# Kernel tuning notes

Measured on AMD Instinct MI355X. Metric: run time of the kernel, lower is better.

The kernel has to match this reference:

```python
import jax, jax.numpy as jnp
import numpy as np

R = 32
EPS = 0.0
BN_EPS = 1e-5


def _voxelize(features, idx):
    # features: [C, N], idx: [N] int32 flat voxel index in [0, R^3)
    V = R * R * R
    pts = features.T  # [N, C]
    sums = jax.ops.segment_sum(pts, idx, num_segments=V)          # [V, C]
    cnts = jax.ops.segment_sum(jnp.ones_like(idx, jnp.float32), idx, num_segments=V)  # [V]
    avg = sums / jnp.maximum(cnts, 1.0)[:, None]
    mx = jax.ops.segment_max(pts, idx, num_segments=V)            # [V, C], -inf for empty
    mx = jnp.where(cnts[:, None] > 0, mx, 0.0)
    return avg, mx, cnts


def reference(features, coords, conv_w, conv_b, bn_gamma, bn_beta, bn_mean, bn_var):
    B, C, N = features.shape
    # --- coordinate normalization (coords detached in original) ---
    nc = coords - jnp.mean(coords, axis=2, keepdims=True)          # [B,3,N]
    norms = jnp.linalg.norm(nc, axis=1, keepdims=True)             # [B,1,N]
    denom = jnp.max(norms, axis=2, keepdims=True) * 2.0 + EPS      # [B,1,1]
    nc = nc / denom + 0.5
    nc = jnp.clip(nc * R, 0.0, R - 1)                              # [B,3,N]
    vox = jnp.round(nc).astype(jnp.int32)                          # [B,3,N]
    idx = vox[:, 0] * (R * R) + vox[:, 1] * R + vox[:, 2]          # [B,N]
    # --- dual scatter reduction (avg + max) per batch ---
    avg, mx, _ = jax.vmap(_voxelize)(features, idx)                # [B, V, C] each
    fea = jnp.concatenate([mx, avg], axis=-1)                      # [B, V, 2C]
    # --- 1x1 Conv3d == channel matmul ---
    y = jnp.einsum('bvc,oc->bvo', fea, conv_w) + conv_b            # [B, V, C]
    # --- BatchNorm3d (eval mode) ---
    y = (y - bn_mean) * (bn_gamma / jnp.sqrt(bn_var + BN_EPS)) + bn_beta
    # --- Swish ---
    y = y * jax.nn.sigmoid(y)
    out = jnp.transpose(y, (0, 2, 1)).reshape(B, C, R, R, R)
    return out, nc


def setup_inputs() -> dict:
    key = jax.random.key(0)
    ks = jax.random.split(key, 8)
    B, C, N = 8, 240, 16384
    return {
        'features': jax.random.normal(ks[0], (B, C, N), jnp.float32),
        'coords': jax.random.normal(ks[1], (B, 3, N), jnp.float32),
        'conv_w': jax.random.normal(ks[2], (C, 2 * C), jnp.float32) * 0.05,
        'conv_b': jax.random.normal(ks[3], (C,), jnp.float32) * 0.05,
        'bn_gamma': jnp.ones((C,), jnp.float32),
        'bn_beta': jnp.zeros((C,), jnp.float32),
        'bn_mean': jnp.zeros((C,), jnp.float32),
        'bn_var': jax.random.uniform(ks[4], (C,), jnp.float32, 0.5, 1.5),
    }
```

## Files before the change

### kernel.cpp

```cpp
#include <hip/hip_runtime.h>
#include <math.h>

#define RR 32
#define V 32768
#define C 240
#define N 16384
#define B 8
#define K2C 480
#define NCOL 1024
#define FPAD 488
#define EBUF 512

typedef __attribute__((ext_vector_type(8))) short bf16x8;
typedef __attribute__((ext_vector_type(4))) float f32x4;

__device__ __forceinline__ unsigned short f2bf(float x) {
    unsigned u = __float_as_uint(x);
    u += 0x7fffu + ((u >> 16) & 1u);
    return (unsigned short)(u >> 16);
}

__global__ __launch_bounds__(1024) void stats_kernel(const float* __restrict__ coords,
                                                     float* __restrict__ stats,
                                                     int* __restrict__ hist,
                                                     const float* __restrict__ w,
                                                     unsigned short* __restrict__ w_bf) {
    int b = blockIdx.x, tid = threadIdx.x;
    int4 z4 = {0, 0, 0, 0};
    int4* hz = (int4*)(hist + b * V);
    for (int i = tid; i < V / 4; i += 1024) hz[i] = z4;
    for (int i = tid; i < 14400; i += 1024) {
        int g = b * 14400 + i;
        w_bf[g] = f2bf(w[g]);
    }
    const float* cb = coords + (size_t)b * 3 * N;
    __shared__ float red[1024];
    float m[3];
    for (int d = 0; d < 3; ++d) {
        float s = 0.f;
        for (int n = tid; n < N; n += 1024) s += cb[d * N + n];
        red[tid] = s; __syncthreads();
        for (int w2 = 512; w2 > 0; w2 >>= 1) { if (tid < w2) red[tid] += red[tid + w2]; __syncthreads(); }
        m[d] = red[0] / (float)N;
        __syncthreads();
    }
    float mx = 0.f;
    for (int n = tid; n < N; n += 1024) {
        float dx = cb[0 * N + n] - m[0];
        float dy = cb[1 * N + n] - m[1];
        float dz = cb[2 * N + n] - m[2];
        mx = fmaxf(mx, dx * dx + dy * dy + dz * dz);
    }
    red[tid] = mx; __syncthreads();
    for (int w2 = 512; w2 > 0; w2 >>= 1) { if (tid < w2) red[tid] = fmaxf(red[tid], red[tid + w2]); __syncthreads(); }
    if (tid == 0) {
        stats[b * 4 + 0] = m[0];
        stats[b * 4 + 1] = m[1];
        stats[b * 4 + 2] = m[2];
        stats[b * 4 + 3] = 2.f * sqrtf(red[0]);
    }
}

__global__ __launch_bounds__(256) void nc_idx_kernel(const float* __restrict__ coords,
                                                     const float* __restrict__ stats,
                                                     float* __restrict__ nc_out,
                                                     int* __restrict__ idxbuf,
                                                     int* __restrict__ hist) {
    int t = blockIdx.x * 256 + threadIdx.x;
    int b = t >> 14;
    int n = t & (N - 1);
    float denom = stats[b * 4 + 3];
    int v[3];
#pragma unroll
    for (int d = 0; d < 3; ++d) {
        float x = coords[((size_t)b * 3 + d) * N + n];
        float t0 = (x - stats[b * 4 + d]) / denom + 0.5f;
        t0 = t0 * (float)RR;
        t0 = fminf(fmaxf(t0, 0.f), (float)(RR - 1));
        nc_out[((size_t)b * 3 + d) * N + n] = t0;
        v[d] = (int)rintf(t0);
    }
    int iv = v[0] * (RR * RR) + v[1] * RR + v[2];
    idxbuf[t] = iv;
    atomicAdd(hist + b * V + iv, 1);
}

__global__ __launch_bounds__(1024) void prefix_kernel(const int* __restrict__ hist,
                                                      int* __restrict__ starts,
                                                      int* __restrict__ cursor) {
    __shared__ int part[1024];
    int b = blockIdx.x, t = threadIdx.x;
    int base = b * V + t * 32;
    const int4* hp = (const int4*)(hist + base);
    int4 h[8];
    int s = 0;
#pragma unroll
    for (int j = 0; j < 8; ++j) { h[j] = hp[j]; s += h[j].x + h[j].y + h[j].z + h[j].w; }
    part[t] = s; __syncthreads();
    for (int off = 1; off < 1024; off <<= 1) {
        int x = (t >= off) ? part[t - off] : 0;
        __syncthreads();
        part[t] += x;
        __syncthreads();
    }
    int run = part[t] - s;
    int4* sp = (int4*)(starts + base);
    int4* cp = (int4*)(cursor + base);
#pragma unroll
    for (int j = 0; j < 8; ++j) {
        int4 o;
        o.x = run; run += h[j].x;
        o.y = run; run += h[j].y;
        o.z = run; run += h[j].z;
        o.w = run; run += h[j].w;
        sp[j] = o; cp[j] = o;
    }
}

__global__ __launch_bounds__(256) void plist_kernel(const int* __restrict__ idxbuf,
                                                    int* __restrict__ cursor,
                                                    int* __restrict__ ptlist) {
    int t = blockIdx.x * 256 + threadIdx.x;
    int b = t >> 14;
    int n = t & (N - 1);
    int iv = idxbuf[t];
    int pos = atomicAdd(cursor + b * V + iv, 1);
    ptlist[(b << 14) + pos] = (n << 5) | (iv & 31);
}

__global__ __launch_bounds__(256) void transpose_kernel(const float* __restrict__ feat,
                                                        unsigned short* __restrict__ featT) {
    __shared__ float t[C][33];
    int b = blockIdx.y;
    int n0 = blockIdx.x * 32;
    int l = threadIdx.x;
    const float* fb = feat + (size_t)b * C * N;
    unsigned short* fTb = featT + (size_t)b * N * C;
    int nl = l & 31, cs = l >> 5;
#pragma unroll
    for (int p = 0; p < 30; ++p) {
        int c = p * 8 + cs;
        t[c][nl] = fb[(size_t)c * N + n0 + nl];
    }
    __syncthreads();
    int ci = l & 127;
    int nh = l >> 7;
#pragma unroll
    for (int p = 0; p < 16; ++p) {
        int n = 2 * p + nh;
        if (ci < 120) {
            unsigned lo = f2bf(t[2 * ci][n]);
            unsigned hi = f2bf(t[2 * ci + 1][n]);
            *(unsigned*)&fTb[(size_t)(n0 + n) * C + 2 * ci] = lo | (hi << 16);
        }
    }
}

__global__ __launch_bounds__(256) void column_kernel(
    const unsigned short* __restrict__ featT,
    const int* __restrict__ ptlist,
    const int* __restrict__ starts,
    const int* __restrict__ hist,
    const unsigned short* __restrict__ w_bf,
    const float* __restrict__ cbias, const float* __restrict__ gamma,
    const float* __restrict__ beta, const float* __restrict__ mean,
    const float* __restrict__ var,
    float* __restrict__ out) {
    const int col = blockIdx.x, b = blockIdx.y;
    const int tid = threadIdx.x;
    const int v0 = col * 32;
    float* outb = out + (size_t)b * C * V;

    __shared__ float A_s[C], B_s[C];
    __shared__ unsigned short fea_s[32][FPAD];
    __shared__ int cnt_s[32];
    __shared__ int ebuf[EBUF];

    if (tid < C) {
        float sc = gamma[tid] * rsqrtf(var[tid] + 1e-5f);
        A_s[tid] = sc;
        B_s[tid] = (cbias[tid] - mean[tid]) * sc + beta[tid];
    }
    if (tid < 32) cnt_s[tid] = hist[b * V + v0 + tid];
    __syncthreads();

    int pc = 0;
#pragma unroll
    for (int z = 0; z < 32; ++z) pc += cnt_s[z];

    if (pc == 0) {
        for (int i = tid; i < C * 32; i += 256) {
            int o = i >> 5, vv = i & 31;
            float y = B_s[o];
            y = y / (1.f + __expf(-y));
            outb[(size_t)o * V + v0 + vv] = y;
        }
        return;
    }

    for (int i = tid; i < 32 * FPAD / 2; i += 256) ((unsigned*)fea_s)[i] = 0u;

    const int cu = tid;
    const bool act = tid < 120;
    const int pos = starts[b * V + v0];
    const int* pl = ptlist + (b << 14) + pos;
    const unsigned short* fT = featT + (size_t)b * N * C;

    float s0 = 0.f, s1 = 0.f, mx0 = -INFINITY, mx1 = -INFINITY;
    int curz = -1;
    for (int base = 0; base < pc; base += EBUF) {
        int mm = min(EBUF, pc - base);
        __syncthreads();
        for (int i = tid; i < mm; i += 256) ebuf[i] = pl[base + i];
        __syncthreads();
        if (act) {
            for (int i0 = 0; i0 < mm; i0 += 16) {
                int m = min(16, mm - i0);
                int e_[16];
#pragma unroll
                for (int j = 0; j < 16; ++j) e_[j] = ebuf[i0 + ((j < m) ? j : m - 1)];
                unsigned u_[16];
#pragma unroll
                for (int j = 0; j < 16; ++j)
                    u_[j] = *(const unsigned*)&fT[(size_t)(e_[j] >> 5) * C + 2 * cu];
#pragma unroll
                for (int j = 0; j < 16; ++j) {
                    if (j < m) {
                        int zj = e_[j] & 31;
                        if (zj != curz) {
                            if (curz >= 0) {
                                float k = (float)cnt_s[curz];
                                unsigned pm = (unsigned)f2bf(mx0) | ((unsigned)f2bf(mx1) << 16);
                                unsigned pa = (unsigned)f2bf(s0 / k) | ((unsigned)f2bf(s1 / k) << 16);
                                *(unsigned*)&fea_s[curz][2 * cu] = pm;
                                *(unsigned*)&fea_s[curz][C + 2 * cu] = pa;
                            }
                            curz = zj; s0 = s1 = 0.f; mx0 = mx1 = -INFINITY;
                        }
                        float lo = __uint_as_float(u_[j] << 16);
                        float hi = __uint_as_float(u_[j] & 0xffff0000u);
                        s0 += lo; s1 += hi;
                        mx0 = fmaxf(mx0, lo); mx1 = fmaxf(mx1, hi);
                    }
                }
            }
        }
    }
    if (act && curz >= 0) {
        float k = (float)cnt_s[curz];
        *(unsigned*)&fea_s[curz][2 * cu] = (unsigned)f2bf(mx0) | ((unsigned)f2bf(mx1) << 16);
        *(unsigned*)&fea_s[curz][C + 2 * cu] = (unsigned)f2bf(s0 / k) | ((unsigned)f2bf(s1 / k) << 16);
    }
    __syncthreads();

    const int lane = tid & 63, wave = tid >> 6;
    const int nt = wave & 1;
    const int mbase = (wave >> 1) * 8;
    const int mcnt = (wave >> 1) ? 7 : 8;
    const int zl = nt * 16 + (lane & 15);
    const int koff = (lane >> 4) * 8;

    f32x4 acc[8];
#pragma unroll
    for (int i = 0; i < 8; ++i) acc[i] = (f32x4){0.f, 0.f, 0.f, 0.f};

#pragma unroll
    for (int kc = 0; kc < 15; ++kc) {
        const int kg = kc * 32 + koff;
        bf16x8 bfr = *(const bf16x8*)&fea_s[zl][kg];
        const unsigned short* wp = w_bf + (size_t)(mbase * 16 + (lane & 15)) * K2C + kg;
#pragma unroll
        for (int mt = 0; mt < 8; ++mt) {
            if (mt < mcnt) {
                bf16x8 afr = *(const bf16x8*)(wp + (size_t)mt * 16 * K2C);
                acc[mt] = __builtin_amdgcn_mfma_f32_16x16x32_bf16(afr, bfr, acc[mt], 0, 0, 0);
            }
        }
    }

    const int vv = v0 + zl;
    const int rbase = (lane >> 4) * 4;
#pragma unroll
    for (int mt = 0; mt < 8; ++mt) {
        if (mt < mcnt) {
#pragma unroll
            for (int r = 0; r < 4; ++r) {
                int o = (mbase + mt) * 16 + rbase + r;
                float y = acc[mt][r] * A_s[o] + B_s[o];
                y = y / (1.f + __expf(-y));
                outb[(size_t)o * V + vv] = y;
            }
        }
    }
}

extern "C" void kernel_launch(void* const* d_in, const int* in_sizes, int n_in,
                              void* d_out, int out_size, void* d_ws, size_t ws_size,
                              hipStream_t stream) {
    const float* features = (const float*)d_in[0];
    const float* coords   = (const float*)d_in[1];
    const float* conv_w   = (const float*)d_in[2];
    const float* conv_b   = (const float*)d_in[3];
    const float* gamma    = (const float*)d_in[4];
    const float* beta     = (const float*)d_in[5];
    const float* mean     = (const float*)d_in[6];
    const float* var      = (const float*)d_in[7];

    float* out    = (float*)d_out;
    float* nc_out = out + (size_t)B * C * V;

    char* ws = (char*)d_ws;
    size_t off = 0;
    auto carve = [&](size_t bytes) { char* p = ws + off; off += (bytes + 255) & ~(size_t)255; return p; };
    int*            hist   = (int*)carve((size_t)B * V * 4);
    float*          stats  = (float*)carve(B * 4 * 4);
    int*            idxbuf = (int*)carve((size_t)B * N * 4);
    int*            starts = (int*)carve((size_t)B * V * 4);
    int*            cursor = (int*)carve((size_t)B * V * 4);
    int*            ptlist = (int*)carve((size_t)B * N * 4);
    unsigned short* w_bf   = (unsigned short*)carve((size_t)C * K2C * 2);
    unsigned short* featT  = (unsigned short*)carve((size_t)B * N * C * 2);
    (void)off;

    stats_kernel<<<B, 1024, 0, stream>>>(coords, stats, hist, conv_w, w_bf);
    nc_idx_kernel<<<(B * N) / 256, 256, 0, stream>>>(coords, stats, nc_out, idxbuf, hist);
    prefix_kernel<<<B, 1024, 0, stream>>>(hist, starts, cursor);
    plist_kernel<<<(B * N) / 256, 256, 0, stream>>>(idxbuf, cursor, ptlist);
    transpose_kernel<<<dim3(N / 32, B), 256, 0, stream>>>(features, featT);
    column_kernel<<<dim3(NCOL, B), 256, 0, stream>>>(
        featT, ptlist, starts, hist, w_bf,
        conv_b, gamma, beta, mean, var, out);
    (void)in_sizes; (void)n_in; (void)out_size;
}
```

Measured before the change: 635.7 us.

## Halve voxel group per block, one channel per thread, parallelize init kernel

The column kernel now handles 16 voxels per block instead of 32, doubling the grid. The gather uses one channel per thread (240 active threads instead of 120 each handling two), and averages use a precomputed reciprocal in place of a division. The MFMA stage now gives each wave 4 output tiles over a single 16-voxel tile, where before it was 8 tiles over two voxel tiles. Separately, histogram zeroing and weight conversion move to 256 wide blocks beside the 8 stats blocks, aiming to cut serial setup time. The trade-off is that weight fragments are reloaded per block twice as often and output stores cover 16 contiguous voxels rather than 32.

```diff
diff --git a/kernel.cpp b/kernel.cpp
--- a/kernel.cpp
+++ b/kernel.cpp
@@ -7,7 +7,8 @@
 #define N 16384
 #define B 8
 #define K2C 480
-#define NCOL 1024
+#define NG 2048
+#define GZ 16
 #define FPAD 488
 #define EBUF 512
 
@@ -20,39 +21,45 @@
     return (unsigned short)(u >> 16);
 }
 
-__global__ __launch_bounds__(1024) void stats_kernel(const float* __restrict__ coords,
-                                                     float* __restrict__ stats,
-                                                     int* __restrict__ hist,
-                                                     const float* __restrict__ w,
-                                                     unsigned short* __restrict__ w_bf) {
-    int b = blockIdx.x, tid = threadIdx.x;
-    int4 z4 = {0, 0, 0, 0};
-    int4* hz = (int4*)(hist + b * V);
-    for (int i = tid; i < V / 4; i += 1024) hz[i] = z4;
-    for (int i = tid; i < 14400; i += 1024) {
-        int g = b * 14400 + i;
-        w_bf[g] = f2bf(w[g]);
-    }
+__global__ __launch_bounds__(256) void init_stats_kernel(const float* __restrict__ coords,
+                                                         float* __restrict__ stats,
+                                                         int* __restrict__ hist,
+                                                         const float* __restrict__ w,
+                                                         unsigned short* __restrict__ w_bf) {
+    int blk = blockIdx.x;
+    int tid = threadIdx.x;
+    if (blk < 256) {
+        int t = blk * 256 + tid;
+        int4 z4 = {0, 0, 0, 0};
+        ((int4*)hist)[t] = z4;
+        if (t < 57600) {
+            unsigned lo = f2bf(w[2 * t]);
+            unsigned hi = f2bf(w[2 * t + 1]);
+            ((unsigned*)w_bf)[t] = lo | (hi << 16);
+        }
+        return;
+    }
+    int b = blk - 256;
     const float* cb = coords + (size_t)b * 3 * N;
-    __shared__ float red[1024];
+    __shared__ float red[256];
     float m[3];
     for (int d = 0; d < 3; ++d) {
         float s = 0.f;
-        for (int n = tid; n < N; n += 1024) s += cb[d * N + n];
+        for (int n = tid; n < N; n += 256) s += cb[d * N + n];
         red[tid] = s; __syncthreads();
-        for (int w2 = 512; w2 > 0; w2 >>= 1) { if (tid < w2) red[tid] += red[tid + w2]; __syncthreads(); }
+        for (int w2 = 128; w2 > 0; w2 >>= 1) { if (tid < w2) red[tid] += red[tid + w2]; __syncthreads(); }
         m[d] = red[0] / (float)N;
         __syncthreads();
     }
     float mx = 0.f;
-    for (int n = tid; n < N; n += 1024) {
+    for (int n = tid; n < N; n += 256) {
         float dx = cb[0 * N + n] - m[0];
         float dy = cb[1 * N + n] - m[1];
         float dz = cb[2 * N + n] - m[2];
         mx = fmaxf(mx, dx * dx + dy * dy + dz * dz);
     }
     red[tid] = mx; __syncthreads();
-    for (int w2 = 512; w2 > 0; w2 >>= 1) { if (tid < w2) red[tid] = fmaxf(red[tid], red[tid + w2]); __syncthreads(); }
+    for (int w2 = 128; w2 > 0; w2 >>= 1) { if (tid < w2) red[tid] = fmaxf(red[tid], red[tid + w2]); __syncthreads(); }
     if (tid == 0) {
         stats[b * 4 + 0] = m[0];
         stats[b * 4 + 1] = m[1];
@@ -166,14 +173,14 @@
     const float* __restrict__ beta, const float* __restrict__ mean,
     const float* __restrict__ var,
     float* __restrict__ out) {
-    const int col = blockIdx.x, b = blockIdx.y;
+    const int g = blockIdx.x, b = blockIdx.y;
     const int tid = threadIdx.x;
-    const int v0 = col * 32;
+    const int v0 = g * GZ;
     float* outb = out + (size_t)b * C * V;
 
-    __shared__ float A_s[C], B_s[C];
-    __shared__ unsigned short fea_s[32][FPAD];
-    __shared__ int cnt_s[32];
+    __shared__ float A_s[C], B_s[C], rcp_s[GZ];
+    __shared__ unsigned short fea_s[GZ][FPAD];
+    __shared__ int cnt_s[GZ];
     __shared__ int ebuf[EBUF];
 
     if (tid < C) {
@@ -181,16 +188,20 @@
         A_s[tid] = sc;
         B_s[tid] = (cbias[tid] - mean[tid]) * sc + beta[tid];
     }
-    if (tid < 32) cnt_s[tid] = hist[b * V + v0 + tid];
+    if (tid < GZ) {
+        int c0 = hist[b * V + v0 + tid];
+        cnt_s[tid] = c0;
+        rcp_s[tid] = 1.f / (float)max(c0, 1);
+    }
     __syncthreads();
 
     int pc = 0;
 #pragma unroll
-    for (int z = 0; z < 32; ++z) pc += cnt_s[z];
+    for (int z = 0; z < GZ; ++z) pc += cnt_s[z];
 
     if (pc == 0) {
-        for (int i = tid; i < C * 32; i += 256) {
-            int o = i >> 5, vv = i & 31;
+        for (int i = tid; i < C * GZ; i += 256) {
+            int o = i >> 4, vv = i & (GZ - 1);
             float y = B_s[o];
             y = y / (1.f + __expf(-y));
             outb[(size_t)o * V + v0 + vv] = y;
@@ -198,15 +209,15 @@
         return;
     }
 
-    for (int i = tid; i < 32 * FPAD / 2; i += 256) ((unsigned*)fea_s)[i] = 0u;
-
-    const int cu = tid;
-    const bool act = tid < 120;
+    for (int i = tid; i < GZ * FPAD / 2; i += 256) ((unsigned*)fea_s)[i] = 0u;
+
+    const int c = tid;
+    const bool act = tid < C;
     const int pos = starts[b * V + v0];
     const int* pl = ptlist + (b << 14) + pos;
     const unsigned short* fT = featT + (size_t)b * N * C;
 
-    float s0 = 0.f, s1 = 0.f, mx0 = -INFINITY, mx1 = -INFINITY;
+    float s0 = 0.f, mx0 = -INFINITY;
     int curz = -1;
     for (int base = 0; base < pc; base += EBUF) {
         int mm = min(EBUF, pc - base);
@@ -219,58 +230,50 @@
                 int e_[16];
 #pragma unroll
                 for (int j = 0; j < 16; ++j) e_[j] = ebuf[i0 + ((j < m) ? j : m - 1)];
-                unsigned u_[16];
+                unsigned short u_[16];
 #pragma unroll
                 for (int j = 0; j < 16; ++j)
-                    u_[j] = *(const unsigned*)&fT[(size_t)(e_[j] >> 5) * C + 2 * cu];
+                    u_[j] = fT[(size_t)(e_[j] >> 5) * C + c];
 #pragma unroll
                 for (int j = 0; j < 16; ++j) {
                     if (j < m) {
-                        int zj = e_[j] & 31;
+                        int zj = e_[j] & (GZ - 1);
                         if (zj != curz) {
                             if (curz >= 0) {
-                                float k = (float)cnt_s[curz];
-                                unsigned pm = (unsigned)f2bf(mx0) | ((unsigned)f2bf(mx1) << 16);
-                                unsigned pa = (unsigned)f2bf(s0 / k) | ((unsigned)f2bf(s1 / k) << 16);
-                                *(unsigned*)&fea_s[curz][2 * cu] = pm;
-                                *(unsigned*)&fea_s[curz][C + 2 * cu] = pa;
+                                fea_s[curz][c] = f2bf(mx0);
+                                fea_s[curz][C + c] = f2bf(s0 * rcp_s[curz]);
                             }
-                            curz = zj; s0 = s1 = 0.f; mx0 = mx1 = -INFINITY;
+                            curz = zj; s0 = 0.f; mx0 = -INFINITY;
                         }
-                        float lo = __uint_as_float(u_[j] << 16);
-                        float hi = __uint_as_float(u_[j] & 0xffff0000u);
-                        s0 += lo; s1 += hi;
-                        mx0 = fmaxf(mx0, lo); mx1 = fmaxf(mx1, hi);
+                        float f = __uint_as_float(((unsigned)u_[j]) << 16);
+                        s0 += f; mx0 = fmaxf(mx0, f);
                     }
                 }
             }
         }
     }
     if (act && curz >= 0) {
-        float k = (float)cnt_s[curz];
-        *(unsigned*)&fea_s[curz][2 * cu] = (unsigned)f2bf(mx0) | ((unsigned)f2bf(mx1) << 16);
-        *(unsigned*)&fea_s[curz][C + 2 * cu] = (unsigned)f2bf(s0 / k) | ((unsigned)f2bf(s1 / k) << 16);
+        fea_s[curz][c] = f2bf(mx0);
+        fea_s[curz][C + c] = f2bf(s0 * rcp_s[curz]);
     }
     __syncthreads();
 
     const int lane = tid & 63, wave = tid >> 6;
-    const int nt = wave & 1;
-    const int mbase = (wave >> 1) * 8;
-    const int mcnt = (wave >> 1) ? 7 : 8;
-    const int zl = nt * 16 + (lane & 15);
+    const int mcnt = (wave == 3) ? 3 : 4;
+    const int zl = lane & 15;
     const int koff = (lane >> 4) * 8;
 
-    f32x4 acc[8];
-#pragma unroll
-    for (int i = 0; i < 8; ++i) acc[i] = (f32x4){0.f, 0.f, 0.f, 0.f};
+    f32x4 acc[4];
+#pragma unroll
+    for (int i = 0; i < 4; ++i) acc[i] = (f32x4){0.f, 0.f, 0.f, 0.f};
 
 #pragma unroll
     for (int kc = 0; kc < 15; ++kc) {
         const int kg = kc * 32 + koff;
         bf16x8 bfr = *(const bf16x8*)&fea_s[zl][kg];
-        const unsigned short* wp = w_bf + (size_t)(mbase * 16 + (lane & 15)) * K2C + kg;
-#pragma unroll
-        for (int mt = 0; mt < 8; ++mt) {
+        const unsigned short* wp = w_bf + (size_t)(wave * 64 + zl) * K2C + kg;
+#pragma unroll
+        for (int mt = 0; mt < 4; ++mt) {
             if (mt < mcnt) {
                 bf16x8 afr = *(const bf16x8*)(wp + (size_t)mt * 16 * K2C);
                 acc[mt] = __builtin_amdgcn_mfma_f32_16x16x32_bf16(afr, bfr, acc[mt], 0, 0, 0);
@@ -281,11 +284,11 @@
     const int vv = v0 + zl;
     const int rbase = (lane >> 4) * 4;
 #pragma unroll
-    for (int mt = 0; mt < 8; ++mt) {
+    for (int mt = 0; mt < 4; ++mt) {
         if (mt < mcnt) {
 #pragma unroll
             for (int r = 0; r < 4; ++r) {
-                int o = (mbase + mt) * 16 + rbase + r;
+                int o = (wave * 4 + mt) * 16 + rbase + r;
                 float y = acc[mt][r] * A_s[o] + B_s[o];
                 y = y / (1.f + __expf(-y));
                 outb[(size_t)o * V + vv] = y;
@@ -322,12 +325,12 @@
     unsigned short* featT  = (unsigned short*)carve((size_t)B * N * C * 2);
     (void)off;
 
-    stats_kernel<<<B, 1024, 0, stream>>>(coords, stats, hist, conv_w, w_bf);
+    init_stats_kernel<<<256 + B, 256, 0, stream>>>(coords, stats, hist, conv_w, w_bf);
     nc_idx_kernel<<<(B * N) / 256, 256, 0, stream>>>(coords, stats, nc_out, idxbuf, hist);
     prefix_kernel<<<B, 1024, 0, stream>>>(hist, starts, cursor);
     plist_kernel<<<(B * N) / 256, 256, 0, stream>>>(idxbuf, cursor, ptlist);
     transpose_kernel<<<dim3(N / 32, B), 256, 0, stream>>>(features, featT);
-    column_kernel<<<dim3(NCOL, B), 256, 0, stream>>>(
+    column_kernel<<<dim3(NG, B), 256, 0, stream>>>(
         featT, ptlist, starts, hist, w_bf,
         conv_b, gamma, beta, mean, var, out);
     (void)in_sizes; (void)n_in; (void)out_size;
```

After: 608.8 us. 4.2% less time.
